# Optimization experiments

Measured on AMD Instinct MI355X. Metric: run time of the kernel, lower is better.

The kernel has to match this reference:

```python
import math
import jax, jax.numpy as jnp
import numpy as np

# Model dims (from Weatherformer defaults: hidden = 8 heads * factor 8 = 64)
B, S, E, H, L = 8, 1024, 64, 8, 3
HD = E // H          # head_dim = 8
FF = 4 * E           # feedforward = 256
IN = 31              # input_dim (weather features)
OUT = 31             # output_dim
NG = 31              # granularity embedding table size
EPS = 1e-5


def setup_inputs() -> dict:
    key = jax.random.key(0)
    ks = jax.random.split(key, 12)
    p = lambda k, shape: jax.random.normal(k, shape, jnp.float32) * 0.05
    return {
        "weather": jax.random.normal(ks[0], (B, S, IN), jnp.float32),
        "coords": jax.random.uniform(ks[1], (B, 2), jnp.float32, -90.0, 90.0),
        "temporal_index": jax.random.randint(ks[2], (B, 2), 0, NG),
        "W_emb": p(ks[3], (IN, E)), "b_emb": jnp.zeros((E,), jnp.float32),
        "W_qkv": p(ks[4], (L, E, 3 * E)), "b_qkv": jnp.zeros((L, 3 * E), jnp.float32),
        "W_out": p(ks[5], (L, E, E)), "b_out": jnp.zeros((L, E), jnp.float32),
        "gran": p(ks[6], (L, NG, E)),
        "g1": jnp.ones((L, E), jnp.float32), "be1": jnp.zeros((L, E), jnp.float32),
        "W1": p(ks[7], (L, E, FF)), "b1": jnp.zeros((L, FF), jnp.float32),
        "W2": p(ks[8], (L, FF, E)), "b2": jnp.zeros((L, E), jnp.float32),
        "g2": jnp.ones((L, E), jnp.float32), "be2": jnp.zeros((L, E), jnp.float32),
        "W_fc": p(ks[9], (E, OUT)), "b_fc": jnp.zeros((OUT,), jnp.float32),
    }


def _layernorm(x, g, b):
    m = jnp.mean(x, axis=-1, keepdims=True)
    v = jnp.var(x, axis=-1, keepdims=True)
    return (x - m) / jnp.sqrt(v + EPS) * g + b


def _pos_encoding(coords):
    # div_term over every 4th channel: [E/4]
    div = jnp.exp(jnp.arange(0, E, 4, dtype=jnp.float32) * (-math.log(10000.0) / E))
    lat = coords[:, :1] / 180.0 * math.pi   # [B,1]
    lon = coords[:, 1:] / 180.0 * math.pi   # [B,1]
    tf = jnp.arange(S, dtype=jnp.float32)[:, None] * div          # [S, E/4]
    q = E // 4
    sin_tf = jnp.broadcast_to(jnp.sin(tf)[None], (B, S, q))       # channels 0::4
    cos_tf = jnp.broadcast_to(jnp.cos(tf)[None], (B, S, q))       # channels 1::4
    sin_lat = jnp.broadcast_to(jnp.sin(lat * div)[:, None, :], (B, S, q))  # 2::4
    cos_lon = jnp.broadcast_to(jnp.cos(lon * div)[:, None, :], (B, S, q))  # 3::4
    return jnp.stack([sin_tf, cos_tf, sin_lat, cos_lon], axis=-1).reshape(B, S, E)


def _attention(x, tg, W_qkv, b_qkv, W_out, b_out, gran_table):
    # Faithful replication of torch's (seq-major) qkv reshape quirk.
    qkv = x @ W_qkv + b_qkv                                  # [B,S,3E]
    qkv = qkv.reshape(B, S, 3, E).transpose(2, 0, 1, 3)      # [3,B,S,E]
    qkv = qkv.reshape(3, S, B * H, HD).transpose(0, 2, 1, 3) # [3,B*H,S,HD]
    q, k, v = qkv[0], qkv[1], qkv[2]
    ge = gran_table[tg].reshape(B * H, 1, HD)                # [B*H,1,HD]
    q = q + ge
    k = k + ge
    scores = jnp.einsum('bqd,bkd->bqk', q, k) * (HD ** -0.5) # [B*H,S,S]
    w = jax.nn.softmax(scores, axis=-1)                      # dropout = identity (eval)
    o = jnp.einsum('bqk,bkd->bqd', w, v)                     # [B*H,S,HD]
    o = o.transpose(1, 0, 2).reshape(B * S, E)
    return (o @ W_out + b_out).reshape(B, S, E)


def reference(weather, coords, temporal_index, W_emb, b_emb, W_qkv, b_qkv,
              W_out, b_out, gran, g1, be1, W1, b1, W2, b2, g2, be2, W_fc, b_fc):
    tg = temporal_index[:, 1:][:, :, None].astype(jnp.int32)  # [B,1,1]
    x = weather @ W_emb + b_emb                               # [B,S,E]
    x = x + _pos_encoding(coords)
    for l in range(L):
        a = _attention(x, tg, W_qkv[l], b_qkv[l], W_out[l], b_out[l], gran[l])
        x = _layernorm(x + a, g1[l], be1[l])
        ff = jax.nn.relu(x @ W1[l] + b1[l]) @ W2[l] + b2[l]
        x = _layernorm(x + ff, g2[l], be2[l])
    return x @ W_fc + b_fc                                    # [B,S,OUT]
```

## Files before the change

kernel.cpp:

```cpp
#include <hip/hip_runtime.h>
#include <math.h>

#define EPS 1e-5f

typedef float f32x16 __attribute__((ext_vector_type(16)));
typedef short short8 __attribute__((ext_vector_type(8)));

union U4S8 { uint4 u; short8 s; };

__device__ __forceinline__ float wave_sum64(float v) {
#pragma unroll
  for (int off = 32; off >= 1; off >>= 1) v += __shfl_xor(v, off, 64);
  return v;
}

__device__ __forceinline__ unsigned int bf16rne(float f) {
  unsigned int u = __float_as_uint(f);
  return (u + 0x7fffu + ((u >> 16) & 1u)) >> 16;
}
__device__ __forceinline__ unsigned int cvt_pk_bf16(float lo, float hi) {
  unsigned int r;
  asm("v_cvt_pk_bf16_f32 %0, %1, %2" : "=v"(r) : "v"(lo), "v"(hi));
  return r;
}

__global__ __launch_bounds__(256) void k_embed(
    const float* __restrict__ weather, const float* __restrict__ coords,
    const float* __restrict__ W_emb, const float* __restrict__ b_emb,
    float* __restrict__ x) {
  int t = threadIdx.x, r = t >> 6, e = t & 63;
  int row = (blockIdx.x << 2) | r;
  int b = row >> 10, s = row & 1023;
  __shared__ float wrow[4][32];
  if (e < 31) wrow[r][e] = weather[row * 31 + e];
  __syncthreads();
  float acc = b_emb[e];
#pragma unroll
  for (int i = 0; i < 31; ++i) acc = fmaf(wrow[r][i], W_emb[i * 64 + e], acc);
  int g = e >> 2, rem = e & 3;
  float div = __expf(-0.5756462732485115f * (float)g);
  float pe;
  if (rem == 0)      pe = sinf((float)s * div);
  else if (rem == 1) pe = cosf((float)s * div);
  else if (rem == 2) pe = sinf(coords[b * 2 + 0] * 0.017453292519943295f * div);
  else               pe = cosf(coords[b * 2 + 1] * 0.017453292519943295f * div);
  x[row * 64 + e] = acc + pe;
}

__global__ __launch_bounds__(192) void k_qkv(
    const float* __restrict__ x, const float* __restrict__ Wq,
    const float* __restrict__ bq, const float* __restrict__ gran,
    const int* __restrict__ tidx, unsigned int* __restrict__ qb,
    unsigned int* __restrict__ kbuf, unsigned short* __restrict__ vt) {
  int t = threadIdx.x;
  int row0 = blockIdx.x << 3;
  float acc[8];
  float bias = bq[t];
#pragma unroll
  for (int r = 0; r < 8; ++r) acc[r] = bias;
  const float* xp = x + (size_t)row0 * 64;
#pragma unroll 4
  for (int k4 = 0; k4 < 16; ++k4) {
    float4 xv[8];
#pragma unroll
    for (int r = 0; r < 8; ++r) xv[r] = *(const float4*)(xp + r * 64 + k4 * 4);
    float w0 = Wq[(4 * k4 + 0) * 192 + t];
    float w1 = Wq[(4 * k4 + 1) * 192 + t];
    float w2 = Wq[(4 * k4 + 2) * 192 + t];
    float w3 = Wq[(4 * k4 + 3) * 192 + t];
#pragma unroll
    for (int r = 0; r < 8; ++r) {
      acc[r] = fmaf(xv[r].x, w0, acc[r]);
      acc[r] = fmaf(xv[r].y, w1, acc[r]);
      acc[r] = fmaf(xv[r].z, w2, acc[r]);
      acc[r] = fmaf(xv[r].w, w3, acc[r]);
    }
  }
  int cq = t & 63;
  int hh = cq >> 3, hd = t & 7;
  int b = row0 >> 10, shi = (row0 & 1023) >> 3;
  int s2 = (b << 7) | shi;
  const float scl = 0.35355339059327373f;
#pragma unroll
  for (int r = 0; r < 8; ++r) {
    float o = acc[r];
    if (t < 128) o += gran[tidx[2 * r + 1] * 64 + cq];
    int bh = (r << 3) | hh;
    if (t < 64) {
      o *= scl;
      float nb = __shfl_down(o, 1, 64);
      if ((hd & 1) == 0)
        qb[((((size_t)bh << 10) | s2) << 2) + (hd >> 1)] =
            bf16rne(o) | (bf16rne(nb) << 16);
    } else if (t < 128) {
      float nb = __shfl_down(o, 1, 64);
      if ((hd & 1) == 0)
        kbuf[((((size_t)bh << 10) | s2) << 2) + (hd >> 1)] =
            bf16rne(o) | (bf16rne(nb) << 16);
    } else {
      vt[((size_t)bh << 13) + (hd << 10) + s2] = (unsigned short)bf16rne(o);
    }
  }
}

__global__ __launch_bounds__(512, 2) void k_attn(
    const unsigned int* __restrict__ qb, const unsigned int* __restrict__ kbuf,
    const unsigned short* __restrict__ vt, float* __restrict__ ao) {
  int bh = blockIdx.x >> 3, chunk = blockIdx.x & 7;
  int slo = bh >> 3, h = bh & 7;
  int t = threadIdx.x;
  int l = t & 63, w = t >> 6;
  int grp = w >> 1, kh = w & 1;
  int lq = l & 31, g = l >> 5;
  bool kl = (l < 32);
  bool vl = (lq < 8);
  int q = (chunk << 7) + (grp << 5) + lq;

  U4S8 qf;
  qf.u = make_uint4(0, 0, 0, 0);
  if (kl) qf.u = *(const uint4*)(qb + ((((size_t)bh << 10) + q) << 2));

  const uint4* kp = (const uint4*)(kbuf + ((size_t)bh << 12));
  const unsigned short* vp = vt + ((size_t)bh << 13);

  f32x16 O, Z;
#pragma unroll
  for (int i = 0; i < 16; ++i) { O[i] = 0.f; Z[i] = 0.f; }
  float m = -1e30f, ls = 0.f;

  int kb0 = kh << 4;
  for (int kblk = kb0; kblk < kb0 + 16; ++kblk) {
    U4S8 af;
    af.u = make_uint4(0, 0, 0, 0);
    if (kl) af.u = kp[(kblk << 5) + lq];
    f32x16 S = __builtin_amdgcn_mfma_f32_32x32x16_bf16(af.s, qf.s, Z, 0, 0, 0);

    float mx = S[0];
#pragma unroll
    for (int i = 1; i < 16; ++i) mx = fmaxf(mx, S[i]);
    mx = fmaxf(mx, __shfl_xor(mx, 32, 64));
    if (mx > m + 8.f) {
      float esc = __expf(m - mx);
      ls *= esc;
      O *= esc;
      m = mx;
    }
    float p[16];
#pragma unroll
    for (int i = 0; i < 16; ++i) p[i] = __expf(S[i] - m);
    float s01 = (p[0] + p[1]) + (p[2] + p[3]);
    float s23 = (p[4] + p[5]) + (p[6] + p[7]);
    float s45 = (p[8] + p[9]) + (p[10] + p[11]);
    float s67 = (p[12] + p[13]) + (p[14] + p[15]);
    ls += (s01 + s23) + (s45 + s67);

    unsigned va = cvt_pk_bf16(p[0], p[1]),  vb = cvt_pk_bf16(p[2], p[3]);
    unsigned vc = cvt_pk_bf16(p[4], p[5]),  vd = cvt_pk_bf16(p[6], p[7]);
    unsigned ve = cvt_pk_bf16(p[8], p[9]),  vf = cvt_pk_bf16(p[10], p[11]);
    unsigned vg = cvt_pk_bf16(p[12], p[13]), vh = cvt_pk_bf16(p[14], p[15]);
    unsigned sa = __shfl_xor((int)va, 32, 64), sb = __shfl_xor((int)vb, 32, 64);
    unsigned sc = __shfl_xor((int)vc, 32, 64), sd = __shfl_xor((int)vd, 32, 64);
    unsigned se = __shfl_xor((int)ve, 32, 64), sf = __shfl_xor((int)vf, 32, 64);
    unsigned sg = __shfl_xor((int)vg, 32, 64), sh = __shfl_xor((int)vh, 32, 64);
    U4S8 b1, b2;
    b1.u.x = kl ? va : sc;  b1.u.y = kl ? vb : sd;
    b1.u.z = kl ? sa : vc;  b1.u.w = kl ? sb : vd;
    b2.u.x = kl ? ve : sg;  b2.u.y = kl ? vf : sh;
    b2.u.z = kl ? se : vg;  b2.u.w = kl ? sf : vh;

    U4S8 v1, v2;
    v1.u = make_uint4(0, 0, 0, 0);
    v2.u = make_uint4(0, 0, 0, 0);
    if (vl) {
      const unsigned short* vb8 = vp + (lq << 10) + (kblk << 5) + (g << 3);
      v1.u = *(const uint4*)vb8;
      v2.u = *(const uint4*)(vb8 + 16);
    }
    O = __builtin_amdgcn_mfma_f32_32x32x16_bf16(v1.s, b1.s, O, 0, 0, 0);
    O = __builtin_amdgcn_mfma_f32_32x32x16_bf16(v2.s, b2.s, O, 0, 0, 0);
  }

  ls += __shfl_xor(ls, 32, 64);

  __shared__ float pm[4][64], pl[4][64];
  __shared__ float po[4][64][4];
  if (kh == 0) {
    pm[grp][l] = m;
    pl[grp][l] = ls;
    *(float4*)(&po[grp][l][0]) = make_float4(O[0], O[1], O[2], O[3]);
  }
  __syncthreads();
  if (kh == 1) {
    float mA = pm[grp][l], lsA = pl[grp][l];
    float nm = fmaxf(m, mA);
    float wB = __expf(m - nm), wA = __expf(mA - nm);
    float4 oA = *(const float4*)(&po[grp][l][0]);
    float inv = 1.0f / (ls * wB + lsA * wA);
    int bq = q >> 7, sq = ((q & 127) << 3) | slo;
    float* op = ao + (((size_t)((bq << 10) | sq)) << 6) + (h << 3) + (g << 2);
    *(float4*)op = make_float4((O[0] * wB + oA.x * wA) * inv,
                               (O[1] * wB + oA.y * wA) * inv,
                               (O[2] * wB + oA.z * wA) * inv,
                               (O[3] * wB + oA.w * wA) * inv);
  }
}

__global__ __launch_bounds__(256, 2) void k_fused(
    const float* x_in, const float* __restrict__ ao,
    const float* __restrict__ Wo, const float* __restrict__ bo,
    const float* __restrict__ g1, const float* __restrict__ be1,
    const float* __restrict__ W1, const float* __restrict__ b1,
    const float* __restrict__ W2, const float* __restrict__ b2,
    const float* __restrict__ g2, const float* __restrict__ be2,
    float* x_out) {
  int t = threadIdx.x, w = t >> 6, c = t & 63;
  int ws = w << 2;
  int row0 = (blockIdx.x << 4) + ws;
  __shared__ unsigned int w2b[8192];
  __shared__ float aos[16][64];
  __shared__ float x1s[16][64];
  __shared__ float h1s[16][256];
  for (int i = t; i < 8192; i += 256) {
    float2 f = *(const float2*)(W2 + 2 * i);
    w2b[i] = bf16rne(f.x) | (bf16rne(f.y) << 16);
  }
  float xin[4];
#pragma unroll
  for (int r = 0; r < 4; ++r) {
    aos[ws + r][c] = ao[(size_t)(row0 + r) * 64 + c];
    xin[r] = x_in[(size_t)(row0 + r) * 64 + c];
  }
  float acc[4];
  float bov = bo[c];
#pragma unroll
  for (int r = 0; r < 4; ++r) acc[r] = bov;
#pragma unroll 4
  for (int k4 = 0; k4 < 16; ++k4) {
    float w0 = Wo[(4 * k4 + 0) * 64 + c], w1 = Wo[(4 * k4 + 1) * 64 + c];
    float w2 = Wo[(4 * k4 + 2) * 64 + c], w3 = Wo[(4 * k4 + 3) * 64 + c];
#pragma unroll
    for (int r = 0; r < 4; ++r) {
      float4 av = *(const float4*)(&aos[ws + r][4 * k4]);
      acc[r] = fmaf(av.x, w0, acc[r]);
      acc[r] = fmaf(av.y, w1, acc[r]);
      acc[r] = fmaf(av.z, w2, acc[r]);
      acc[r] = fmaf(av.w, w3, acc[r]);
    }
  }
  float g1v = g1[c], be1v = be1[c];
  float x1v[4];
#pragma unroll
  for (int r = 0; r < 4; ++r) {
    float y = acc[r] + xin[r];
    float s1 = wave_sum64(y), s2 = wave_sum64(y * y);
    float mean = s1 * 0.015625f, var = s2 * 0.015625f - mean * mean;
    x1v[r] = (y - mean) * rsqrtf(var + EPS) * g1v + be1v;
    x1s[ws + r][c] = x1v[r];
  }
  float4 h[4];
  float4 b1v = *(const float4*)(b1 + 4 * c);
#pragma unroll
  for (int r = 0; r < 4; ++r) h[r] = b1v;
#pragma unroll 4
  for (int k4 = 0; k4 < 16; ++k4) {
    float4 w0 = *(const float4*)(W1 + (size_t)(4 * k4 + 0) * 256 + 4 * c);
    float4 w1 = *(const float4*)(W1 + (size_t)(4 * k4 + 1) * 256 + 4 * c);
    float4 w2 = *(const float4*)(W1 + (size_t)(4 * k4 + 2) * 256 + 4 * c);
    float4 w3 = *(const float4*)(W1 + (size_t)(4 * k4 + 3) * 256 + 4 * c);
#pragma unroll
    for (int r = 0; r < 4; ++r) {
      float4 xv = *(const float4*)(&x1s[ws + r][4 * k4]);
      h[r].x = fmaf(xv.x, w0.x, h[r].x); h[r].y = fmaf(xv.x, w0.y, h[r].y);
      h[r].z = fmaf(xv.x, w0.z, h[r].z); h[r].w = fmaf(xv.x, w0.w, h[r].w);
      h[r].x = fmaf(xv.y, w1.x, h[r].x); h[r].y = fmaf(xv.y, w1.y, h[r].y);
      h[r].z = fmaf(xv.y, w1.z, h[r].z); h[r].w = fmaf(xv.y, w1.w, h[r].w);
      h[r].x = fmaf(xv.z, w2.x, h[r].x); h[r].y = fmaf(xv.z, w2.y, h[r].y);
      h[r].z = fmaf(xv.z, w2.z, h[r].z); h[r].w = fmaf(xv.z, w2.w, h[r].w);
      h[r].x = fmaf(xv.w, w3.x, h[r].x); h[r].y = fmaf(xv.w, w3.y, h[r].y);
      h[r].z = fmaf(xv.w, w3.z, h[r].z); h[r].w = fmaf(xv.w, w3.w, h[r].w);
    }
  }
#pragma unroll
  for (int r = 0; r < 4; ++r) {
    h[r].x = fmaxf(h[r].x, 0.f); h[r].y = fmaxf(h[r].y, 0.f);
    h[r].z = fmaxf(h[r].z, 0.f); h[r].w = fmaxf(h[r].w, 0.f);
    *(float4*)(&h1s[ws + r][4 * c]) = h[r];
  }
  __syncthreads();
  int sh = (c & 1) ? 0 : 16;
  int wbase = c >> 1;
  float acc2[4];
  float b2v = b2[c];
#pragma unroll
  for (int r = 0; r < 4; ++r) acc2[r] = b2v;
#pragma unroll 4
  for (int k4 = 0; k4 < 64; ++k4) {
    float w0 = __uint_as_float((w2b[(4 * k4 + 0) * 32 + wbase] << sh) & 0xffff0000u);
    float w1 = __uint_as_float((w2b[(4 * k4 + 1) * 32 + wbase] << sh) & 0xffff0000u);
    float w2 = __uint_as_float((w2b[(4 * k4 + 2) * 32 + wbase] << sh) & 0xffff0000u);
    float w3 = __uint_as_float((w2b[(4 * k4 + 3) * 32 + wbase] << sh) & 0xffff0000u);
#pragma unroll
    for (int r = 0; r < 4; ++r) {
      float4 hv = *(const float4*)(&h1s[ws + r][4 * k4]);
      acc2[r] = fmaf(hv.x, w0, acc2[r]);
      acc2[r] = fmaf(hv.y, w1, acc2[r]);
      acc2[r] = fmaf(hv.z, w2, acc2[r]);
      acc2[r] = fmaf(hv.w, w3, acc2[r]);
    }
  }
  float g2v = g2[c], be2v = be2[c];
#pragma unroll
  for (int r = 0; r < 4; ++r) {
    float y2 = acc2[r] + x1v[r];
    float t1 = wave_sum64(y2), t2 = wave_sum64(y2 * y2);
    float mean2 = t1 * 0.015625f, var2 = t2 * 0.015625f - mean2 * mean2;
    x_out[(size_t)(row0 + r) * 64 + c] =
        (y2 - mean2) * rsqrtf(var2 + EPS) * g2v + be2v;
  }
}

__global__ __launch_bounds__(256) void k_head(
    const float* __restrict__ x, const float* __restrict__ Wfc,
    const float* __restrict__ bfc, float* __restrict__ out) {
  int gid = blockIdx.x * 256 + threadIdx.x;
  int r = gid >> 5, o = gid & 31;
  if (o >= 31) return;
  float acc = bfc[o];
  const float* xr = x + (size_t)r * 64;
#pragma unroll
  for (int i = 0; i < 64; ++i) acc = fmaf(xr[i], Wfc[i * 31 + o], acc);
  out[(size_t)r * 31 + o] = acc;
}

extern "C" void kernel_launch(void* const* d_in, const int* in_sizes, int n_in,
                              void* d_out, int out_size, void* d_ws, size_t ws_size,
                              hipStream_t stream) {
  const float* weather = (const float*)d_in[0];
  const float* coords  = (const float*)d_in[1];
  const int*   tidx    = (const int*)d_in[2];
  const float* W_emb   = (const float*)d_in[3];
  const float* b_emb   = (const float*)d_in[4];
  const float* W_qkv   = (const float*)d_in[5];
  const float* b_qkv   = (const float*)d_in[6];
  const float* W_out   = (const float*)d_in[7];
  const float* b_out   = (const float*)d_in[8];
  const float* gran    = (const float*)d_in[9];
  const float* g1      = (const float*)d_in[10];
  const float* be1     = (const float*)d_in[11];
  const float* W1      = (const float*)d_in[12];
  const float* b1      = (const float*)d_in[13];
  const float* W2      = (const float*)d_in[14];
  const float* b2      = (const float*)d_in[15];
  const float* g2      = (const float*)d_in[16];
  const float* be2     = (const float*)d_in[17];
  const float* W_fc    = (const float*)d_in[18];
  const float* b_fc    = (const float*)d_in[19];
  float* out = (float*)d_out;

  float* x = (float*)d_ws;
  unsigned int* qbw = (unsigned int*)(x + 8192 * 64);
  unsigned int* kbw = qbw + 64 * 1024 * 4;
  unsigned short* vtw = (unsigned short*)(kbw + 64 * 1024 * 4);
  float* ao = (float*)(vtw + 64 * 8 * 1024);

  k_embed<<<2048, 256, 0, stream>>>(weather, coords, W_emb, b_emb, x);
  for (int l = 0; l < 3; ++l) {
    k_qkv<<<1024, 192, 0, stream>>>(x, W_qkv + l * 64 * 192, b_qkv + l * 192,
                                    gran + l * 31 * 64, tidx, qbw, kbw, vtw);
    k_attn<<<512, 512, 0, stream>>>(qbw, kbw, vtw, ao);
    k_fused<<<512, 256, 0, stream>>>(x, ao, W_out + l * 64 * 64, b_out + l * 64,
                                     g1 + l * 64, be1 + l * 64,
                                     W1 + l * 64 * 256, b1 + l * 256,
                                     W2 + l * 256 * 64, b2 + l * 64,
                                     g2 + l * 64, be2 + l * 64, x);
  }
  k_head<<<1024, 256, 0, stream>>>(x, W_fc, b_fc, out);
}
```

Before: 184.0 us.

## Fuse embedding into first QKV kernel and next-layer QKV into fused FFN

```diff
diff --git a/kernel.cpp b/kernel.cpp
--- a/kernel.cpp
+++ b/kernel.cpp
@@ -24,46 +24,52 @@
   return r;
 }
 
-__global__ __launch_bounds__(256) void k_embed(
+__global__ __launch_bounds__(192) void k_qkv0(
     const float* __restrict__ weather, const float* __restrict__ coords,
     const float* __restrict__ W_emb, const float* __restrict__ b_emb,
-    float* __restrict__ x) {
-  int t = threadIdx.x, r = t >> 6, e = t & 63;
-  int row = (blockIdx.x << 2) | r;
-  int b = row >> 10, s = row & 1023;
-  __shared__ float wrow[4][32];
-  if (e < 31) wrow[r][e] = weather[row * 31 + e];
-  __syncthreads();
-  float acc = b_emb[e];
-#pragma unroll
-  for (int i = 0; i < 31; ++i) acc = fmaf(wrow[r][i], W_emb[i * 64 + e], acc);
-  int g = e >> 2, rem = e & 3;
-  float div = __expf(-0.5756462732485115f * (float)g);
-  float pe;
-  if (rem == 0)      pe = sinf((float)s * div);
-  else if (rem == 1) pe = cosf((float)s * div);
-  else if (rem == 2) pe = sinf(coords[b * 2 + 0] * 0.017453292519943295f * div);
-  else               pe = cosf(coords[b * 2 + 1] * 0.017453292519943295f * div);
-  x[row * 64 + e] = acc + pe;
-}
-
-__global__ __launch_bounds__(192) void k_qkv(
-    const float* __restrict__ x, const float* __restrict__ Wq,
-    const float* __restrict__ bq, const float* __restrict__ gran,
-    const int* __restrict__ tidx, unsigned int* __restrict__ qb,
+    const float* __restrict__ Wq, const float* __restrict__ bq,
+    const float* __restrict__ gran, const int* __restrict__ tidx,
+    float* __restrict__ x, unsigned int* __restrict__ qb,
     unsigned int* __restrict__ kbuf, unsigned short* __restrict__ vt) {
   int t = threadIdx.x;
   int row0 = blockIdx.x << 3;
+  __shared__ float wrow[8][32];
+  __shared__ float xs[8][64];
+  for (int i = t; i < 256; i += 192) {
+    int r = i >> 5, c2 = i & 31;
+    if (c2 < 31) wrow[r][c2] = weather[(size_t)(row0 + r) * 31 + c2];
+  }
+  __syncthreads();
+  int b = row0 >> 10;
+  float lat = coords[b * 2 + 0] * 0.017453292519943295f;
+  float lon = coords[b * 2 + 1] * 0.017453292519943295f;
+  for (int idx = t; idx < 512; idx += 192) {
+    int r = idx >> 6, e = idx & 63;
+    int s = (row0 + r) & 1023;
+    float acc = b_emb[e];
+#pragma unroll
+    for (int i = 0; i < 31; ++i) acc = fmaf(wrow[r][i], W_emb[i * 64 + e], acc);
+    int g = e >> 2, rem = e & 3;
+    float div = __expf(-0.5756462732485115f * (float)g);
+    float pe;
+    if (rem == 0)      pe = sinf((float)s * div);
+    else if (rem == 1) pe = cosf((float)s * div);
+    else if (rem == 2) pe = sinf(lat * div);
+    else               pe = cosf(lon * div);
+    float xv = acc + pe;
+    xs[r][e] = xv;
+    x[(size_t)(row0 + r) * 64 + e] = xv;
+  }
+  __syncthreads();
   float acc[8];
   float bias = bq[t];
 #pragma unroll
   for (int r = 0; r < 8; ++r) acc[r] = bias;
-  const float* xp = x + (size_t)row0 * 64;
 #pragma unroll 4
   for (int k4 = 0; k4 < 16; ++k4) {
     float4 xv[8];
 #pragma unroll
-    for (int r = 0; r < 8; ++r) xv[r] = *(const float4*)(xp + r * 64 + k4 * 4);
+    for (int r = 0; r < 8; ++r) xv[r] = *(const float4*)(&xs[r][4 * k4]);
     float w0 = Wq[(4 * k4 + 0) * 192 + t];
     float w1 = Wq[(4 * k4 + 1) * 192 + t];
     float w2 = Wq[(4 * k4 + 2) * 192 + t];
@@ -78,7 +84,7 @@
   }
   int cq = t & 63;
   int hh = cq >> 3, hd = t & 7;
-  int b = row0 >> 10, shi = (row0 & 1023) >> 3;
+  int shi = (row0 & 1023) >> 3;
   int s2 = (b << 7) | shi;
   const float scl = 0.35355339059327373f;
 #pragma unroll
@@ -196,8 +202,8 @@
     float wB = __expf(m - nm), wA = __expf(mA - nm);
     float4 oA = *(const float4*)(&po[grp][l][0]);
     float inv = 1.0f / (ls * wB + lsA * wA);
-    int bq = q >> 7, sq = ((q & 127) << 3) | slo;
-    float* op = ao + (((size_t)((bq << 10) | sq)) << 6) + (h << 3) + (g << 2);
+    int bq2 = q >> 7, sq = ((q & 127) << 3) | slo;
+    float* op = ao + (((size_t)((bq2 << 10) | sq)) << 6) + (h << 3) + (g << 2);
     *(float4*)op = make_float4((O[0] * wB + oA.x * wA) * inv,
                                (O[1] * wB + oA.y * wA) * inv,
                                (O[2] * wB + oA.z * wA) * inv,
@@ -205,6 +211,7 @@
   }
 }
 
+template <bool EMIT>
 __global__ __launch_bounds__(256, 2) void k_fused(
     const float* x_in, const float* __restrict__ ao,
     const float* __restrict__ Wo, const float* __restrict__ bo,
@@ -212,10 +219,14 @@
     const float* __restrict__ W1, const float* __restrict__ b1,
     const float* __restrict__ W2, const float* __restrict__ b2,
     const float* __restrict__ g2, const float* __restrict__ be2,
-    float* x_out) {
+    const float* __restrict__ Wq, const float* __restrict__ bq,
+    const float* __restrict__ gran, const int* __restrict__ tidx,
+    unsigned int* __restrict__ qbo, unsigned int* __restrict__ kbo,
+    unsigned short* __restrict__ vto, float* __restrict__ x_out) {
   int t = threadIdx.x, w = t >> 6, c = t & 63;
   int ws = w << 2;
-  int row0 = (blockIdx.x << 4) + ws;
+  int row_base = blockIdx.x << 4;
+  int row0 = row_base + ws;
   __shared__ unsigned int w2b[8192];
   __shared__ float aos[16][64];
   __shared__ float x1s[16][64];
@@ -288,17 +299,17 @@
   }
   __syncthreads();
   int sh = (c & 1) ? 0 : 16;
-  int wbase = c >> 1;
+  int wb2 = c >> 1;
   float acc2[4];
   float b2v = b2[c];
 #pragma unroll
   for (int r = 0; r < 4; ++r) acc2[r] = b2v;
 #pragma unroll 4
   for (int k4 = 0; k4 < 64; ++k4) {
-    float w0 = __uint_as_float((w2b[(4 * k4 + 0) * 32 + wbase] << sh) & 0xffff0000u);
-    float w1 = __uint_as_float((w2b[(4 * k4 + 1) * 32 + wbase] << sh) & 0xffff0000u);
-    float w2 = __uint_as_float((w2b[(4 * k4 + 2) * 32 + wbase] << sh) & 0xffff0000u);
-    float w3 = __uint_as_float((w2b[(4 * k4 + 3) * 32 + wbase] << sh) & 0xffff0000u);
+    float w0 = __uint_as_float((w2b[(4 * k4 + 0) * 32 + wb2] << sh) & 0xffff0000u);
+    float w1 = __uint_as_float((w2b[(4 * k4 + 1) * 32 + wb2] << sh) & 0xffff0000u);
+    float w2 = __uint_as_float((w2b[(4 * k4 + 2) * 32 + wb2] << sh) & 0xffff0000u);
+    float w3 = __uint_as_float((w2b[(4 * k4 + 3) * 32 + wb2] << sh) & 0xffff0000u);
 #pragma unroll
     for (int r = 0; r < 4; ++r) {
       float4 hv = *(const float4*)(&h1s[ws + r][4 * k4]);
@@ -314,8 +325,47 @@
     float y2 = acc2[r] + x1v[r];
     float t1 = wave_sum64(y2), t2 = wave_sum64(y2 * y2);
     float mean2 = t1 * 0.015625f, var2 = t2 * 0.015625f - mean2 * mean2;
-    x_out[(size_t)(row0 + r) * 64 + c] =
-        (y2 - mean2) * rsqrtf(var2 + EPS) * g2v + be2v;
+    float xo = (y2 - mean2) * rsqrtf(var2 + EPS) * g2v + be2v;
+    x_out[(size_t)(row0 + r) * 64 + c] = xo;
+    aos[ws + r][c] = xo;
+  }
+  if (EMIT) {
+    __syncthreads();
+    if (t < 192) {
+      float qa[16];
+      float bias = bq[t];
+#pragma unroll
+      for (int r = 0; r < 16; ++r) qa[r] = bias;
+      for (int k = 0; k < 64; ++k) {
+        float wqv = Wq[k * 192 + t];
+#pragma unroll
+        for (int r = 0; r < 16; ++r) qa[r] = fmaf(aos[r][k], wqv, qa[r]);
+      }
+      int cq = t & 63, hh = cq >> 3, hd = t & 7;
+      int bb = row_base >> 10;
+      const float scl = 0.35355339059327373f;
+#pragma unroll
+      for (int r = 0; r < 16; ++r) {
+        float o = qa[r];
+        if (t < 128) o += gran[tidx[2 * (r & 7) + 1] * 64 + cq];
+        int row = row_base + r;
+        int s2 = (bb << 7) | ((row & 1023) >> 3);
+        int bh = ((r & 7) << 3) | hh;
+        size_t base = ((size_t)(bh << 10)) | s2;
+        if (t < 64) {
+          o *= scl;
+          float nb = __shfl_down(o, 1, 64);
+          if ((hd & 1) == 0)
+            qbo[(base << 2) + (hd >> 1)] = bf16rne(o) | (bf16rne(nb) << 16);
+        } else if (t < 128) {
+          float nb = __shfl_down(o, 1, 64);
+          if ((hd & 1) == 0)
+            kbo[(base << 2) + (hd >> 1)] = bf16rne(o) | (bf16rne(nb) << 16);
+        } else {
+          vto[((size_t)bh << 13) + (hd << 10) + s2] = (unsigned short)bf16rne(o);
+        }
+      }
+    }
   }
 }
 
@@ -363,16 +413,25 @@
   unsigned short* vtw = (unsigned short*)(kbw + 64 * 1024 * 4);
   float* ao = (float*)(vtw + 64 * 8 * 1024);
 
-  k_embed<<<2048, 256, 0, stream>>>(weather, coords, W_emb, b_emb, x);
+  k_qkv0<<<1024, 192, 0, stream>>>(weather, coords, W_emb, b_emb,
+                                   W_qkv, b_qkv, gran, tidx,
+                                   x, qbw, kbw, vtw);
   for (int l = 0; l < 3; ++l) {
-    k_qkv<<<1024, 192, 0, stream>>>(x, W_qkv + l * 64 * 192, b_qkv + l * 192,
-                                    gran + l * 31 * 64, tidx, qbw, kbw, vtw);
     k_attn<<<512, 512, 0, stream>>>(qbw, kbw, vtw, ao);
-    k_fused<<<512, 256, 0, stream>>>(x, ao, W_out + l * 64 * 64, b_out + l * 64,
-                                     g1 + l * 64, be1 + l * 64,
-                                     W1 + l * 64 * 256, b1 + l * 256,
-                                     W2 + l * 256 * 64, b2 + l * 64,
-                                     g2 + l * 64, be2 + l * 64, x);
+    if (l < 2) {
+      k_fused<true><<<512, 256, 0, stream>>>(
+          x, ao, W_out + l * 64 * 64, b_out + l * 64,
+          g1 + l * 64, be1 + l * 64, W1 + l * 64 * 256, b1 + l * 256,
+          W2 + l * 256 * 64, b2 + l * 64, g2 + l * 64, be2 + l * 64,
+          W_qkv + (l + 1) * 64 * 192, b_qkv + (l + 1) * 192,
+          gran + (l + 1) * 31 * 64, tidx, qbw, kbw, vtw, x);
+    } else {
+      k_fused<false><<<512, 256, 0, stream>>>(
+          x, ao, W_out + l * 64 * 64, b_out + l * 64,
+          g1 + l * 64, be1 + l * 64, W1 + l * 64 * 256, b1 + l * 256,
+          W2 + l * 256 * 64, b2 + l * 64, g2 + l * 64, be2 + l * 64,
+          nullptr, nullptr, nullptr, nullptr, nullptr, nullptr, nullptr, x);
+    }
   }
   k_head<<<1024, 256, 0, stream>>>(x, W_fc, b_fc, out);
 }
```

Measured after the change: 175.4 us. 1.05x faster.
